# Kernel optimization log

Measured on AMD Instinct MI355X. Metric: run time of the kernel, lower is better.

The kernel has to match this reference:

```python
import jax, jax.numpy as jnp
import numpy as np

M, N, IN_DIM, NITER = 32, 32, 1024, 100
ALPHA, SIGMA = 0.3, 16.0  # sigma default = max(m, n) / 2
BATCH = 16384


def setup_inputs() -> dict:
    key = jax.random.key(0)
    k1, k2 = jax.random.split(key)
    x = jax.random.normal(k1, (BATCH, IN_DIM), dtype=jnp.float32)
    weights = jax.random.normal(k2, (IN_DIM, M * N), dtype=jnp.float32)
    ii, jj = jnp.meshgrid(jnp.arange(M), jnp.arange(N), indexing='ij')
    locations = jnp.stack([ii.ravel(), jj.ravel()], axis=1).astype(jnp.int32)  # (m*n, 2), row-major like the generator
    return {"x": x, "weights": weights, "locations": locations, "current_iter": 10}


def reference(x, weights, locations, current_iter):
    # x: (B, in_dim); weights: (in_dim, m*n); locations: (m*n, 2)
    B = x.shape[0]
    # Euclidean distances from each sample to each neuron, via ||a-b||^2 expansion
    x2 = jnp.sum(x * x, axis=1, keepdims=True)            # (B, 1)
    w2 = jnp.sum(weights * weights, axis=0)[None, :]      # (1, m*n)
    d2 = jnp.clip(x2 + w2 - 2.0 * (x @ weights), 0.0, None)
    dists = jnp.sqrt(d2)                                  # (B, m*n)
    loss_per = jnp.min(dists, axis=1)                     # (B,)
    bmu_index = jnp.argmin(dists, axis=1)                 # (B,)
    iter_correction = 1.0 - current_iter / NITER
    lr = ALPHA * iter_correction
    sigma = SIGMA * iter_correction
    loc_f = locations.astype(jnp.float32)                 # (m*n, 2)
    bmu_loc = loc_f[bmu_index]                            # (B, 2)
    # squared grid distance of every neuron to each sample's BMU
    dsq = jnp.sum((loc_f[None, :, :] - bmu_loc[:, None, :]) ** 2, axis=2)  # (B, m*n)
    lr_locations = jnp.exp(-dsq / (sigma * sigma)) * lr   # (B, m*n)
    # delta[i,k] = (1/B) * sum_b lr_locations[b,k] * (x[b,i] - weights[i,k])
    # computed without materializing the (B, in_dim, m*n) broadcast tensor
    pos = jnp.einsum('bk,bi->ik', lr_locations, x)        # (in_dim, m*n)
    neg = weights * jnp.sum(lr_locations, axis=0)[None, :]
    delta = (pos - neg) / B
    new_weights = weights + delta
    loss = jnp.sum(loss_per) / B
    return loss, new_weights
```

## Files before the change

kernel.cpp:

```cpp
#include <hip/hip_runtime.h>

typedef unsigned short u16;
typedef short bf16x8 __attribute__((ext_vector_type(8)));
typedef float f32x4 __attribute__((ext_vector_type(4)));

#define BATCH   16384
#define INDIM   1024
#define KNEUR   1024

__device__ __forceinline__ u16 f2bf(float f) {
  union { float f; unsigned u; } v; v.f = f;
  unsigned r = v.u + 0x7FFFu + ((v.u >> 16) & 1u);
  return (u16)(r >> 16);
}
__device__ __forceinline__ float bf2f(u16 h) {
  union { unsigned u; float f; } v; v.u = ((unsigned)h) << 16; return v.f;
}

#define GLDS(gp, lp) __builtin_amdgcn_global_load_lds( \
  (const __attribute__((address_space(1))) void*)(gp), \
  (__attribute__((address_space(3))) void*)(lp), 16, 0, 0)

__global__ void k_T(const int* __restrict__ loc, const int* __restrict__ itp,
                    u16* __restrict__ Tb, float* __restrict__ Tf,
                    float* __restrict__ Xf, int* __restrict__ cntcur,
                    float* __restrict__ S, float* __restrict__ w2) {
  int id = blockIdx.x * 256 + threadIdx.x;
  int c = id >> 10, k = id & 1023;
  float corr = 1.f - (float)itp[0] / 100.f;
  float lr = 0.3f * corr;
  float sig = 16.f * corr;
  float inv_s2 = 1.f / (sig * sig);
  int di = loc[2 * c] - loc[2 * k];
  int dj = loc[2 * c + 1] - loc[2 * k + 1];
  float v = lr * __expf(-(float)(di * di + dj * dj) * inv_s2);
  Tf[id] = v;
  Tb[id] = f2bf(v);
  Xf[id] = 0.f;
  if (id < 2048) cntcur[id] = 0;
  if (id < 1024) { S[id] = 0.f; w2[id] = 0.f; }
}

__global__ void k_conv_x(const float* __restrict__ x, u16* __restrict__ xb,
                         float* __restrict__ x2) {
  int b = blockIdx.x;
  int t = threadIdx.x;
  const float4 v = *(const float4*)(x + (size_t)b * INDIM + t * 4);
  u16 o0 = f2bf(v.x), o1 = f2bf(v.y), o2 = f2bf(v.z), o3 = f2bf(v.w);
  ushort4 o; o.x = o0; o.y = o1; o.z = o2; o.w = o3;
  *(ushort4*)(xb + (size_t)b * INDIM + t * 4) = o;
  float s = v.x * v.x + v.y * v.y + v.z * v.z + v.w * v.w;
  for (int m = 32; m; m >>= 1) s += __shfl_xor(s, m, 64);
  __shared__ float ws_[4];
  if ((t & 63) == 0) ws_[t >> 6] = s;
  __syncthreads();
  if (t == 0) x2[b] = ws_[0] + ws_[1] + ws_[2] + ws_[3];
}

__global__ void k_prepw(const float* __restrict__ w, u16* __restrict__ wt,
                        float* __restrict__ w2) {
  __shared__ float tile[64][65];
  __shared__ float red[4][64];
  int bi = blockIdx.x & 15;
  int bj = blockIdx.x >> 4;
  int tx = threadIdx.x & 63, ty = threadIdx.x >> 6;
  int i0 = bj * 64, k0 = bi * 64;
  float sq = 0.f;
  for (int r = ty; r < 64; r += 4) {
    float v = w[(size_t)(i0 + r) * KNEUR + k0 + tx];
    tile[r][tx] = v;
  }
  __syncthreads();
  for (int r = ty; r < 64; r += 4) {
    float v = tile[r][tx];
    sq += v * v;
  }
  red[ty][tx] = sq;
  for (int r = ty; r < 64; r += 4)
    wt[(size_t)(k0 + r) * INDIM + i0 + tx] = f2bf(tile[tx][r]);
  __syncthreads();
  if (ty == 0)
    atomicAdd(&w2[k0 + tx], red[0][tx] + red[1][tx] + red[2][tx] + red[3][tx]);
}

template <int EPI>
__global__ __launch_bounds__(256, 4)
void k_gemm(const u16* __restrict__ A, const u16* __restrict__ Bm,
            const float* __restrict__ x2, const float* __restrict__ w2,
            float* __restrict__ pmin, int* __restrict__ pidx,
            float* __restrict__ P4) {
  __shared__ __align__(16) u16 ldsA[128 * 64];
  __shared__ __align__(16) u16 ldsB[128 * 64];
  __shared__ float s_rv[2][128];
  __shared__ int   s_ri[2][128];

  int bid = blockIdx.x;
  int mb, nb, ktlo, kthi, ks;
  if (EPI == 1) {
    int swz = (bid & 7) * 128 + (bid >> 3);
    mb = swz >> 3; nb = swz & 7;
    ktlo = 0; kthi = 16; ks = 0;
  } else {
    ks = bid & 3;
    int tile = bid >> 2;
    mb = tile >> 3; nb = tile & 7;
    ktlo = ks * 4; kthi = ktlo + 4;
  }
  int lane = threadIdx.x & 63;
  int wid = threadIdx.x >> 6;
  int wr = wid >> 1, wc = wid & 1;

  f32x4 acc[4][4];
  #pragma unroll
  for (int i = 0; i < 4; ++i)
    #pragma unroll
    for (int j = 0; j < 4; ++j) { acc[i][j][0] = 0.f; acc[i][j][1] = 0.f; acc[i][j][2] = 0.f; acc[i][j][3] = 0.f; }

  const size_t rowA0 = (size_t)mb * 128;
  const size_t rowB0 = (size_t)nb * 128;

  for (int kt = ktlo; kt < kthi; ++kt) {
    int k0 = kt * 64;
    __syncthreads();
    #pragma unroll
    for (int q = 0; q < 4; ++q) {
      int p = q * 256 + wid * 64 + lane;
      int row = p >> 3;
      int clog = (p & 7) ^ (row & 7);
      GLDS(A + (rowA0 + row) * 1024 + k0 + clog * 8,
           ldsA + (size_t)(q * 256 + wid * 64) * 8);
    }
    #pragma unroll
    for (int q = 0; q < 4; ++q) {
      int p = q * 256 + wid * 64 + lane;
      int row = p >> 3;
      int clog = (p & 7) ^ (row & 7);
      GLDS(Bm + (rowB0 + row) * 1024 + k0 + clog * 8,
           ldsB + (size_t)(q * 256 + wid * 64) * 8);
    }
    __syncthreads();
    #pragma unroll
    for (int kk = 0; kk < 2; ++kk) {
      bf16x8 af[4], bfr[4];
      #pragma unroll
      for (int mt = 0; mt < 4; ++mt) {
        int row = wr * 64 + mt * 16 + (lane & 15);
        int ch = (kk * 4 + (lane >> 4)) ^ (row & 7);
        af[mt] = *(const bf16x8*)(ldsA + row * 64 + ch * 8);
      }
      #pragma unroll
      for (int nt = 0; nt < 4; ++nt) {
        int row = wc * 64 + nt * 16 + (lane & 15);
        int ch = (kk * 4 + (lane >> 4)) ^ (row & 7);
        bfr[nt] = *(const bf16x8*)(ldsB + row * 64 + ch * 8);
      }
      #pragma unroll
      for (int mt = 0; mt < 4; ++mt)
        #pragma unroll
        for (int nt = 0; nt < 4; ++nt)
          acc[mt][nt] = __builtin_amdgcn_mfma_f32_16x16x32_bf16(af[mt], bfr[nt], acc[mt][nt], 0, 0, 0);
    }
  }

  if (EPI == 1) {
    int g = lane >> 4;
    int li = lane & 15;
    #pragma unroll
    for (int mt = 0; mt < 4; ++mt) {
      #pragma unroll
      for (int r = 0; r < 4; ++r) {
        int rowl = wr * 64 + mt * 16 + g * 4 + r;
        float xv = x2[rowA0 + rowl];
        float v = 1e30f; int vi = 0;
        #pragma unroll
        for (int nt = 0; nt < 4; ++nt) {
          int col = (int)rowB0 + wc * 64 + nt * 16 + li;
          float d2 = xv + w2[col] - 2.f * acc[mt][nt][r];
          if (d2 < v) { v = d2; vi = col; }
        }
        #pragma unroll
        for (int m = 1; m < 16; m <<= 1) {
          float ov = __shfl_xor(v, m, 64);
          int oi = __shfl_xor(vi, m, 64);
          if (ov < v || (ov == v && oi < vi)) { v = ov; vi = oi; }
        }
        if (li == 0) { s_rv[wc][rowl] = v; s_ri[wc][rowl] = vi; }
      }
    }
    __syncthreads();
    int t = threadIdx.x;
    if (t < 128) {
      float v0 = s_rv[0][t], v1 = s_rv[1][t];
      int i0 = s_ri[0][t], i1 = s_ri[1][t];
      float v = v0; int vi = i0;
      if (v1 < v0) { v = v1; vi = i1; }
      size_t brow = rowA0 + t;
      pmin[brow * 8 + nb] = v;
      pidx[brow * 8 + nb] = vi;
    }
  } else {
    float* base = P4 + ((size_t)ks << 20);
    #pragma unroll
    for (int mt = 0; mt < 4; ++mt)
      #pragma unroll
      for (int nt = 0; nt < 4; ++nt)
        #pragma unroll
        for (int r = 0; r < 4; ++r) {
          int i = (int)rowA0 + wr * 64 + mt * 16 + (lane >> 4) * 4 + r;
          int k = (int)rowB0 + wc * 64 + nt * 16 + (lane & 15);
          base[(size_t)i * KNEUR + k] = acc[mt][nt][r];
        }
  }
}

__global__ void k_bmu_count(const float* __restrict__ pmin, const int* __restrict__ pidx,
                            int* __restrict__ bmu, float* __restrict__ lpart,
                            int* __restrict__ cnt) {
  int b = blockIdx.x * 256 + threadIdx.x;
  float v = 1e30f; int vi = 0;
  #pragma unroll
  for (int j = 0; j < 8; ++j) {
    float pv = pmin[(size_t)b * 8 + j];
    if (pv < v) { v = pv; vi = pidx[(size_t)b * 8 + j]; }
  }
  bmu[b] = vi;
  atomicAdd(&cnt[vi], 1);
  float d = sqrtf(fmaxf(v, 0.f));
  __shared__ float red[256];
  red[threadIdx.x] = d;
  __syncthreads();
  for (int s = 128; s > 0; s >>= 1) {
    if (threadIdx.x < s) red[threadIdx.x] += red[threadIdx.x + s];
    __syncthreads();
  }
  if (threadIdx.x == 0) lpart[blockIdx.x] = red[0];
}

__global__ void k_offsets_loss(const int* __restrict__ cntcur_in, int* __restrict__ cursor,
                               float* __restrict__ cntf,
                               const float* __restrict__ lpart, float* __restrict__ out) {
  __shared__ int s[1024];
  int t = threadIdx.x;
  int v = cntcur_in[t];
  cntf[t] = (float)v;
  s[t] = v;
  __syncthreads();
  for (int off = 1; off < 1024; off <<= 1) {
    int a = s[t];
    int b = (t >= off) ? s[t - off] : 0;
    __syncthreads();
    s[t] = a + b;
    __syncthreads();
  }
  cursor[t] = s[t] - v;
  if (t < 64) {
    float l = lpart[t];
    for (int m = 32; m; m >>= 1) l += __shfl_xor(l, m, 64);
    if (t == 0) out[0] = l * (1.f / (float)BATCH);
  }
}

__global__ void k_place(const int* __restrict__ bmu, int* __restrict__ cursor,
                        int* __restrict__ perm) {
  int b = blockIdx.x * 256 + threadIdx.x;
  int c = bmu[b];
  int p = atomicAdd(&cursor[c], 1);
  perm[p] = b;
}

__global__ __launch_bounds__(256)
void k_xsum2(const int* __restrict__ perm, const int* __restrict__ bmu,
             const u16* __restrict__ xb, float* __restrict__ Xf) {
  int t = threadIdx.x;
  int m0 = blockIdx.x * 16;
  int pm[16], cl[16];
  #pragma unroll
  for (int j = 0; j < 16; ++j) pm[j] = perm[m0 + j];
  #pragma unroll
  for (int j = 0; j < 16; ++j) cl[j] = bmu[pm[j]];
  float a0 = 0.f, a1 = 0.f, a2 = 0.f, a3 = 0.f;
  int ccur = cl[0];
  #pragma unroll
  for (int j = 0; j < 16; ++j) {
    if (cl[j] != ccur) {
      float* p = Xf + (size_t)ccur * INDIM + 4 * t;
      atomicAdd(p + 0, a0); atomicAdd(p + 1, a1);
      atomicAdd(p + 2, a2); atomicAdd(p + 3, a3);
      a0 = a1 = a2 = a3 = 0.f;
      ccur = cl[j];
    }
    ushort4 v = *(const ushort4*)(xb + (size_t)pm[j] * INDIM + t * 4);
    a0 += bf2f(v.x); a1 += bf2f(v.y); a2 += bf2f(v.z); a3 += bf2f(v.w);
  }
  float* p = Xf + (size_t)ccur * INDIM + 4 * t;
  atomicAdd(p + 0, a0); atomicAdd(p + 1, a1);
  atomicAdd(p + 2, a2); atomicAdd(p + 3, a3);
}

__global__ void k_xst_trans(const float* __restrict__ Xf, u16* __restrict__ xst) {
  __shared__ float tile[64][65];
  int bc = blockIdx.x & 15;
  int bi = blockIdx.x >> 4;
  int tx = threadIdx.x & 63, ty = threadIdx.x >> 6;
  int c0 = bc * 64, i0 = bi * 64;
  for (int r = ty; r < 64; r += 4)
    tile[r][tx] = Xf[(size_t)(c0 + r) * INDIM + i0 + tx];
  __syncthreads();
  for (int r = ty; r < 64; r += 4)
    xst[(size_t)(i0 + r) * KNEUR + c0 + tx] = f2bf(tile[tx][r]);
}

__global__ void k_S(const float* __restrict__ cntf, const float* __restrict__ Tf,
                    float* __restrict__ S) {
  int cchunk = blockIdx.x >> 2;
  int kb = blockIdx.x & 3;
  int k = kb * 256 + threadIdx.x;
  float s = 0.f;
  for (int c = cchunk * 64; c < cchunk * 64 + 64; ++c)
    s += cntf[c] * Tf[(size_t)c * KNEUR + k];
  atomicAdd(&S[k], s);
}

__global__ void k_wupd(const float* __restrict__ P4, const float* __restrict__ Wf,
                       const float* __restrict__ S, float* __restrict__ outw) {
  const float invB = 1.f / (float)BATCH;
  int id4 = blockIdx.x * 256 + threadIdx.x;
  size_t base = (size_t)id4 * 4;
  int k = (int)(base & 1023);
  float4 p0 = *(const float4*)(P4 + base);
  float4 p1 = *(const float4*)(P4 + (1u << 20) + base);
  float4 p2 = *(const float4*)(P4 + (2u << 20) + base);
  float4 p3 = *(const float4*)(P4 + (3u << 20) + base);
  float4 wv = *(const float4*)(Wf + base);
  float4 sv = *(const float4*)(S + k);
  outw[base + 0] = wv.x + (p0.x + p1.x + p2.x + p3.x - wv.x * sv.x) * invB;
  outw[base + 1] = wv.y + (p0.y + p1.y + p2.y + p3.y - wv.y * sv.y) * invB;
  outw[base + 2] = wv.z + (p0.z + p1.z + p2.z + p3.z - wv.z * sv.z) * invB;
  outw[base + 3] = wv.w + (p0.w + p1.w + p2.w + p3.w - wv.w * sv.w) * invB;
}

extern "C" void kernel_launch(void* const* d_in, const int* in_sizes, int n_in,
                              void* d_out, int out_size, void* d_ws, size_t ws_size,
                              hipStream_t stream) {
  const float* x = (const float*)d_in[0];
  const float* w = (const float*)d_in[1];
  const int* loc = (const int*)d_in[2];
  const int* it = (const int*)d_in[3];
  float* out = (float*)d_out;

  char* ws = (char*)d_ws;
  size_t off = 0;
  auto alloc = [&](size_t bytes) -> void* {
    void* p = ws + off;
    off += (bytes + 255) & ~(size_t)255;
    return p;
  };
  u16* xb    = (u16*)  alloc((size_t)BATCH * INDIM * 2);
  u16* wt    = (u16*)  alloc((size_t)KNEUR * INDIM * 2);
  u16* Tb    = (u16*)  alloc((size_t)KNEUR * KNEUR * 2);
  float* Tf  = (float*)alloc((size_t)KNEUR * KNEUR * 4);
  u16* xst   = (u16*)  alloc((size_t)INDIM * KNEUR * 2);
  float* x2  = (float*)alloc((size_t)BATCH * 4);
  float* w2  = (float*)alloc((size_t)KNEUR * 4);
  float* pmin= (float*)alloc((size_t)BATCH * 8 * 4);
  int* pidx  = (int*)  alloc((size_t)BATCH * 8 * 4);
  int* bmu   = (int*)  alloc((size_t)BATCH * 4);
  float* cntf= (float*)alloc((size_t)KNEUR * 4);
  float* S   = (float*)alloc((size_t)KNEUR * 4);
  float* lpart=(float*)alloc(64 * 4);
  float* Xf  = (float*)alloc((size_t)KNEUR * INDIM * 4);
  int* cntcur= (int*)  alloc((size_t)2 * KNEUR * 4);
  int* perm  = (int*)  alloc((size_t)BATCH * 4);
  if (off > ws_size) return;

  int* cnt = cntcur;
  int* cursor = cntcur + KNEUR;
  float* P4 = (float*)xb;

  k_T<<<4096, 256, 0, stream>>>(loc, it, Tb, Tf, Xf, cntcur, S, w2);
  k_conv_x<<<BATCH, 256, 0, stream>>>(x, xb, x2);
  k_prepw<<<256, 256, 0, stream>>>(w, wt, w2);
  k_gemm<1><<<1024, 256, 0, stream>>>(xb, wt, x2, w2, pmin, pidx, nullptr);
  k_bmu_count<<<64, 256, 0, stream>>>(pmin, pidx, bmu, lpart, cnt);
  k_offsets_loss<<<1, 1024, 0, stream>>>(cnt, cursor, cntf, lpart, out);
  k_place<<<64, 256, 0, stream>>>(bmu, cursor, perm);
  k_xsum2<<<BATCH / 16, 256, 0, stream>>>(perm, bmu, xb, Xf);
  k_xst_trans<<<256, 256, 0, stream>>>(Xf, xst);
  k_S<<<64, 256, 0, stream>>>(cntf, Tf, S);
  k_gemm<2><<<256, 256, 0, stream>>>(xst, Tb, nullptr, nullptr, nullptr, nullptr, P4);
  k_wupd<<<1024, 256, 0, stream>>>(P4, w, S, out + 1);
}
```

Baseline: 166.8 us.

## Merge prep kernels and middle stages into cooperative kernel, fuse weight update into GEMM

Folds the three prep kernels into one multi-role launch and moves the BMU, scan, place, x-sum, transpose and S stages into a single cooperative kernel that uses grid syncs in place of separate launches. The W*(1-S/B) base term is now written inside the cooperative kernel, and the second GEMM atomically adds its split-K partials scaled by 1/B straight into the output, so the P4 buffer and the final update kernel go away. w2 is now computed by dedicated column-reduction blocks rather than atomics. This removes launch gaps and a large scratch round trip, in exchange for grid-sync cost, float atomics on a 1M-element output, and a requirement that 1024 blocks can be co-resident.

```diff
diff --git a/kernel.cpp b/kernel.cpp
--- a/kernel.cpp
+++ b/kernel.cpp
@@ -1,4 +1,7 @@
 #include <hip/hip_runtime.h>
+#include <hip/hip_cooperative_groups.h>
+
+namespace cg = cooperative_groups;
 
 typedef unsigned short u16;
 typedef short bf16x8 __attribute__((ext_vector_type(8)));
@@ -21,66 +24,68 @@
   (const __attribute__((address_space(1))) void*)(gp), \
   (__attribute__((address_space(3))) void*)(lp), 16, 0, 0)
 
-__global__ void k_T(const int* __restrict__ loc, const int* __restrict__ itp,
-                    u16* __restrict__ Tb, float* __restrict__ Tf,
-                    float* __restrict__ Xf, int* __restrict__ cntcur,
-                    float* __restrict__ S, float* __restrict__ w2) {
-  int id = blockIdx.x * 256 + threadIdx.x;
-  int c = id >> 10, k = id & 1023;
-  float corr = 1.f - (float)itp[0] / 100.f;
-  float lr = 0.3f * corr;
-  float sig = 16.f * corr;
-  float inv_s2 = 1.f / (sig * sig);
-  int di = loc[2 * c] - loc[2 * k];
-  int dj = loc[2 * c + 1] - loc[2 * k + 1];
-  float v = lr * __expf(-(float)(di * di + dj * dj) * inv_s2);
-  Tf[id] = v;
-  Tb[id] = f2bf(v);
-  Xf[id] = 0.f;
-  if (id < 2048) cntcur[id] = 0;
-  if (id < 1024) { S[id] = 0.f; w2[id] = 0.f; }
-}
-
-__global__ void k_conv_x(const float* __restrict__ x, u16* __restrict__ xb,
-                         float* __restrict__ x2) {
-  int b = blockIdx.x;
-  int t = threadIdx.x;
-  const float4 v = *(const float4*)(x + (size_t)b * INDIM + t * 4);
-  u16 o0 = f2bf(v.x), o1 = f2bf(v.y), o2 = f2bf(v.z), o3 = f2bf(v.w);
-  ushort4 o; o.x = o0; o.y = o1; o.z = o2; o.w = o3;
-  *(ushort4*)(xb + (size_t)b * INDIM + t * 4) = o;
-  float s = v.x * v.x + v.y * v.y + v.z * v.z + v.w * v.w;
-  for (int m = 32; m; m >>= 1) s += __shfl_xor(s, m, 64);
-  __shared__ float ws_[4];
-  if ((t & 63) == 0) ws_[t >> 6] = s;
-  __syncthreads();
-  if (t == 0) x2[b] = ws_[0] + ws_[1] + ws_[2] + ws_[3];
-}
-
-__global__ void k_prepw(const float* __restrict__ w, u16* __restrict__ wt,
-                        float* __restrict__ w2) {
+__global__ __launch_bounds__(256)
+void k_prep(const float* __restrict__ x, u16* __restrict__ xb, float* __restrict__ x2,
+            const float* __restrict__ w, u16* __restrict__ wt, float* __restrict__ w2,
+            const int* __restrict__ loc, const int* __restrict__ itp,
+            u16* __restrict__ Tb, float* __restrict__ Tf,
+            float* __restrict__ Xf, int* __restrict__ cntcur) {
   __shared__ float tile[64][65];
   __shared__ float red[4][64];
-  int bi = blockIdx.x & 15;
-  int bj = blockIdx.x >> 4;
-  int tx = threadIdx.x & 63, ty = threadIdx.x >> 6;
-  int i0 = bj * 64, k0 = bi * 64;
-  float sq = 0.f;
-  for (int r = ty; r < 64; r += 4) {
-    float v = w[(size_t)(i0 + r) * KNEUR + k0 + tx];
-    tile[r][tx] = v;
-  }
-  __syncthreads();
-  for (int r = ty; r < 64; r += 4) {
-    float v = tile[r][tx];
-    sq += v * v;
-  }
-  red[ty][tx] = sq;
-  for (int r = ty; r < 64; r += 4)
-    wt[(size_t)(k0 + r) * INDIM + i0 + tx] = f2bf(tile[tx][r]);
-  __syncthreads();
-  if (ty == 0)
-    atomicAdd(&w2[k0 + tx], red[0][tx] + red[1][tx] + red[2][tx] + red[3][tx]);
+  int bid = blockIdx.x;
+  int t = threadIdx.x;
+  if (bid < 4096) {
+    int row = bid * 4 + (t >> 6);
+    int l = t & 63;
+    const float* xr = x + (size_t)row * INDIM;
+    u16* xbr = xb + (size_t)row * INDIM;
+    float s = 0.f;
+    #pragma unroll
+    for (int seg = 0; seg < 4; ++seg) {
+      float4 v = *(const float4*)(xr + seg * 256 + l * 4);
+      ushort4 o; o.x = f2bf(v.x); o.y = f2bf(v.y); o.z = f2bf(v.z); o.w = f2bf(v.w);
+      *(ushort4*)(xbr + seg * 256 + l * 4) = o;
+      s += v.x * v.x + v.y * v.y + v.z * v.z + v.w * v.w;
+    }
+    for (int m = 32; m; m >>= 1) s += __shfl_xor(s, m, 64);
+    if (l == 0) x2[row] = s;
+  } else if (bid < 8192) {
+    int id = (bid - 4096) * 256 + t;
+    int c = id >> 10, k = id & 1023;
+    float corr = 1.f - (float)itp[0] / 100.f;
+    float lr = 0.3f * corr;
+    float sig = 16.f * corr;
+    float inv_s2 = 1.f / (sig * sig);
+    int di = loc[2 * c] - loc[2 * k];
+    int dj = loc[2 * c + 1] - loc[2 * k + 1];
+    float v = lr * __expf(-(float)(di * di + dj * dj) * inv_s2);
+    Tf[id] = v;
+    Tb[id] = f2bf(v);
+    Xf[id] = 0.f;
+    if (id < 2048) cntcur[id] = 0;
+  } else if (bid < 8448) {
+    int bb = bid - 8192;
+    int bi = bb & 15;
+    int bj = bb >> 4;
+    int tx = t & 63, ty = t >> 6;
+    int i0 = bj * 64, k0 = bi * 64;
+    for (int r = ty; r < 64; r += 4)
+      tile[r][tx] = w[(size_t)(i0 + r) * KNEUR + k0 + tx];
+    __syncthreads();
+    for (int r = ty; r < 64; r += 4)
+      wt[(size_t)(k0 + r) * INDIM + i0 + tx] = f2bf(tile[tx][r]);
+  } else {
+    int tx = t & 63, ty = t >> 6;
+    int k = (bid - 8448) * 64 + tx;
+    float s = 0.f;
+    for (int i = ty * 256; i < ty * 256 + 256; ++i) {
+      float v = w[(size_t)i * KNEUR + k];
+      s += v * v;
+    }
+    red[ty][tx] = s;
+    __syncthreads();
+    if (ty == 0) w2[k] = red[0][tx] + red[1][tx] + red[2][tx] + red[3][tx];
+  }
 }
 
 template <int EPI>
@@ -88,20 +93,20 @@
 void k_gemm(const u16* __restrict__ A, const u16* __restrict__ Bm,
             const float* __restrict__ x2, const float* __restrict__ w2,
             float* __restrict__ pmin, int* __restrict__ pidx,
-            float* __restrict__ P4) {
+            float* __restrict__ outw) {
   __shared__ __align__(16) u16 ldsA[128 * 64];
   __shared__ __align__(16) u16 ldsB[128 * 64];
   __shared__ float s_rv[2][128];
   __shared__ int   s_ri[2][128];
 
   int bid = blockIdx.x;
-  int mb, nb, ktlo, kthi, ks;
+  int mb, nb, ktlo, kthi;
   if (EPI == 1) {
     int swz = (bid & 7) * 128 + (bid >> 3);
     mb = swz >> 3; nb = swz & 7;
-    ktlo = 0; kthi = 16; ks = 0;
+    ktlo = 0; kthi = 16;
   } else {
-    ks = bid & 3;
+    int ks = bid & 3;
     int tile = bid >> 2;
     mb = tile >> 3; nb = tile & 7;
     ktlo = ks * 4; kthi = ktlo + 4;
@@ -199,7 +204,7 @@
       pidx[brow * 8 + nb] = vi;
     }
   } else {
-    float* base = P4 + ((size_t)ks << 20);
+    const float invB = 1.f / (float)BATCH;
     #pragma unroll
     for (int mt = 0; mt < 4; ++mt)
       #pragma unroll
@@ -208,135 +213,138 @@
         for (int r = 0; r < 4; ++r) {
           int i = (int)rowA0 + wr * 64 + mt * 16 + (lane >> 4) * 4 + r;
           int k = (int)rowB0 + wc * 64 + nt * 16 + (lane & 15);
-          base[(size_t)i * KNEUR + k] = acc[mt][nt][r];
+          atomicAdd(&outw[(size_t)i * KNEUR + k], acc[mt][nt][r] * invB);
         }
   }
 }
 
-__global__ void k_bmu_count(const float* __restrict__ pmin, const int* __restrict__ pidx,
-                            int* __restrict__ bmu, float* __restrict__ lpart,
-                            int* __restrict__ cnt) {
-  int b = blockIdx.x * 256 + threadIdx.x;
-  float v = 1e30f; int vi = 0;
-  #pragma unroll
-  for (int j = 0; j < 8; ++j) {
-    float pv = pmin[(size_t)b * 8 + j];
-    if (pv < v) { v = pv; vi = pidx[(size_t)b * 8 + j]; }
-  }
-  bmu[b] = vi;
-  atomicAdd(&cnt[vi], 1);
-  float d = sqrtf(fmaxf(v, 0.f));
-  __shared__ float red[256];
-  red[threadIdx.x] = d;
-  __syncthreads();
-  for (int s = 128; s > 0; s >>= 1) {
-    if (threadIdx.x < s) red[threadIdx.x] += red[threadIdx.x + s];
-    __syncthreads();
-  }
-  if (threadIdx.x == 0) lpart[blockIdx.x] = red[0];
-}
-
-__global__ void k_offsets_loss(const int* __restrict__ cntcur_in, int* __restrict__ cursor,
-                               float* __restrict__ cntf,
-                               const float* __restrict__ lpart, float* __restrict__ out) {
-  __shared__ int s[1024];
+__global__ __launch_bounds__(256, 4)
+void k_coop(const float* __restrict__ pmin, const int* __restrict__ pidx,
+            int* __restrict__ bmu, float* __restrict__ lpart,
+            int* __restrict__ cnt, int* __restrict__ cursor,
+            float* __restrict__ cntf, float* __restrict__ out,
+            const u16* __restrict__ xb, int* __restrict__ perm,
+            float* __restrict__ Xf, u16* __restrict__ xst,
+            const float* __restrict__ Tf, float* __restrict__ S,
+            const float* __restrict__ w, float* __restrict__ outw) {
+  cg::grid_group grid = cg::this_grid();
+  int bid = blockIdx.x;
   int t = threadIdx.x;
-  int v = cntcur_in[t];
-  cntf[t] = (float)v;
-  s[t] = v;
-  __syncthreads();
-  for (int off = 1; off < 1024; off <<= 1) {
-    int a = s[t];
-    int b = (t >= off) ? s[t - off] : 0;
-    __syncthreads();
-    s[t] = a + b;
-    __syncthreads();
-  }
-  cursor[t] = s[t] - v;
-  if (t < 64) {
-    float l = lpart[t];
-    for (int m = 32; m; m >>= 1) l += __shfl_xor(l, m, 64);
-    if (t == 0) out[0] = l * (1.f / (float)BATCH);
-  }
-}
-
-__global__ void k_place(const int* __restrict__ bmu, int* __restrict__ cursor,
-                        int* __restrict__ perm) {
-  int b = blockIdx.x * 256 + threadIdx.x;
-  int c = bmu[b];
-  int p = atomicAdd(&cursor[c], 1);
-  perm[p] = b;
-}
-
-__global__ __launch_bounds__(256)
-void k_xsum2(const int* __restrict__ perm, const int* __restrict__ bmu,
-             const u16* __restrict__ xb, float* __restrict__ Xf) {
-  int t = threadIdx.x;
-  int m0 = blockIdx.x * 16;
-  int pm[16], cl[16];
-  #pragma unroll
-  for (int j = 0; j < 16; ++j) pm[j] = perm[m0 + j];
-  #pragma unroll
-  for (int j = 0; j < 16; ++j) cl[j] = bmu[pm[j]];
-  float a0 = 0.f, a1 = 0.f, a2 = 0.f, a3 = 0.f;
-  int ccur = cl[0];
-  #pragma unroll
-  for (int j = 0; j < 16; ++j) {
-    if (cl[j] != ccur) {
-      float* p = Xf + (size_t)ccur * INDIM + 4 * t;
-      atomicAdd(p + 0, a0); atomicAdd(p + 1, a1);
-      atomicAdd(p + 2, a2); atomicAdd(p + 3, a3);
-      a0 = a1 = a2 = a3 = 0.f;
-      ccur = cl[j];
-    }
-    ushort4 v = *(const ushort4*)(xb + (size_t)pm[j] * INDIM + t * 4);
-    a0 += bf2f(v.x); a1 += bf2f(v.y); a2 += bf2f(v.z); a3 += bf2f(v.w);
-  }
-  float* p = Xf + (size_t)ccur * INDIM + 4 * t;
-  atomicAdd(p + 0, a0); atomicAdd(p + 1, a1);
-  atomicAdd(p + 2, a2); atomicAdd(p + 3, a3);
-}
-
-__global__ void k_xst_trans(const float* __restrict__ Xf, u16* __restrict__ xst) {
   __shared__ float tile[64][65];
-  int bc = blockIdx.x & 15;
-  int bi = blockIdx.x >> 4;
-  int tx = threadIdx.x & 63, ty = threadIdx.x >> 6;
-  int c0 = bc * 64, i0 = bi * 64;
-  for (int r = ty; r < 64; r += 4)
-    tile[r][tx] = Xf[(size_t)(c0 + r) * INDIM + i0 + tx];
-  __syncthreads();
-  for (int r = ty; r < 64; r += 4)
-    xst[(size_t)(i0 + r) * KNEUR + c0 + tx] = f2bf(tile[tx][r]);
-}
-
-__global__ void k_S(const float* __restrict__ cntf, const float* __restrict__ Tf,
-                    float* __restrict__ S) {
-  int cchunk = blockIdx.x >> 2;
-  int kb = blockIdx.x & 3;
-  int k = kb * 256 + threadIdx.x;
-  float s = 0.f;
-  for (int c = cchunk * 64; c < cchunk * 64 + 64; ++c)
-    s += cntf[c] * Tf[(size_t)c * KNEUR + k];
-  atomicAdd(&S[k], s);
-}
-
-__global__ void k_wupd(const float* __restrict__ P4, const float* __restrict__ Wf,
-                       const float* __restrict__ S, float* __restrict__ outw) {
-  const float invB = 1.f / (float)BATCH;
-  int id4 = blockIdx.x * 256 + threadIdx.x;
-  size_t base = (size_t)id4 * 4;
-  int k = (int)(base & 1023);
-  float4 p0 = *(const float4*)(P4 + base);
-  float4 p1 = *(const float4*)(P4 + (1u << 20) + base);
-  float4 p2 = *(const float4*)(P4 + (2u << 20) + base);
-  float4 p3 = *(const float4*)(P4 + (3u << 20) + base);
-  float4 wv = *(const float4*)(Wf + base);
-  float4 sv = *(const float4*)(S + k);
-  outw[base + 0] = wv.x + (p0.x + p1.x + p2.x + p3.x - wv.x * sv.x) * invB;
-  outw[base + 1] = wv.y + (p0.y + p1.y + p2.y + p3.y - wv.y * sv.y) * invB;
-  outw[base + 2] = wv.z + (p0.z + p1.z + p2.z + p3.z - wv.z * sv.z) * invB;
-  outw[base + 3] = wv.w + (p0.w + p1.w + p2.w + p3.w - wv.w * sv.w) * invB;
+
+  if (bid < 64) {
+    int b = bid * 256 + t;
+    float v = 1e30f; int vi = 0;
+    #pragma unroll
+    for (int j = 0; j < 8; ++j) {
+      float pv = pmin[(size_t)b * 8 + j];
+      if (pv < v) { v = pv; vi = pidx[(size_t)b * 8 + j]; }
+    }
+    bmu[b] = vi;
+    atomicAdd(&cnt[vi], 1);
+    float d = sqrtf(fmaxf(v, 0.f));
+    __shared__ float red[256];
+    red[t] = d;
+    __syncthreads();
+    for (int s = 128; s > 0; s >>= 1) {
+      if (t < s) red[t] += red[t + s];
+      __syncthreads();
+    }
+    if (t == 0) lpart[bid] = red[0];
+  }
+  grid.sync();
+
+  if (bid == 0) {
+    __shared__ int sc[256];
+    int4 c4 = *(const int4*)(cnt + 4 * t);
+    int tsum = c4.x + c4.y + c4.z + c4.w;
+    sc[t] = tsum;
+    __syncthreads();
+    for (int off = 1; off < 256; off <<= 1) {
+      int val = sc[t];
+      int add = (t >= off) ? sc[t - off] : 0;
+      __syncthreads();
+      sc[t] = val + add;
+      __syncthreads();
+    }
+    int excl = sc[t] - tsum;
+    cursor[4 * t + 0] = excl;
+    cursor[4 * t + 1] = excl + c4.x;
+    cursor[4 * t + 2] = excl + c4.x + c4.y;
+    cursor[4 * t + 3] = excl + c4.x + c4.y + c4.z;
+    cntf[4 * t + 0] = (float)c4.x;
+    cntf[4 * t + 1] = (float)c4.y;
+    cntf[4 * t + 2] = (float)c4.z;
+    cntf[4 * t + 3] = (float)c4.w;
+    if (t < 64) {
+      float l = lpart[t];
+      for (int m = 32; m; m >>= 1) l += __shfl_xor(l, m, 64);
+      if (t == 0) out[0] = l * (1.f / (float)BATCH);
+    }
+  }
+  grid.sync();
+
+  if (bid < 64) {
+    int b = bid * 256 + t;
+    int c = bmu[b];
+    int p = atomicAdd(&cursor[c], 1);
+    perm[p] = b;
+  } else if (bid < 68) {
+    int k = (bid - 64) * 256 + t;
+    float s = 0.f;
+    for (int c = 0; c < KNEUR; ++c)
+      s += cntf[c] * Tf[(size_t)c * KNEUR + k];
+    S[k] = s;
+  }
+  grid.sync();
+
+  {
+    int m0 = bid * 16;
+    int pm[16], cl[16];
+    #pragma unroll
+    for (int j = 0; j < 16; ++j) pm[j] = perm[m0 + j];
+    #pragma unroll
+    for (int j = 0; j < 16; ++j) cl[j] = bmu[pm[j]];
+    float a0 = 0.f, a1 = 0.f, a2 = 0.f, a3 = 0.f;
+    int ccur = cl[0];
+    #pragma unroll
+    for (int j = 0; j < 16; ++j) {
+      if (cl[j] != ccur) {
+        float* p = Xf + (size_t)ccur * INDIM + 4 * t;
+        atomicAdd(p + 0, a0); atomicAdd(p + 1, a1);
+        atomicAdd(p + 2, a2); atomicAdd(p + 3, a3);
+        a0 = a1 = a2 = a3 = 0.f;
+        ccur = cl[j];
+      }
+      ushort4 v = *(const ushort4*)(xb + (size_t)pm[j] * INDIM + t * 4);
+      a0 += bf2f(v.x); a1 += bf2f(v.y); a2 += bf2f(v.z); a3 += bf2f(v.w);
+    }
+    float* p = Xf + (size_t)ccur * INDIM + 4 * t;
+    atomicAdd(p + 0, a0); atomicAdd(p + 1, a1);
+    atomicAdd(p + 2, a2); atomicAdd(p + 3, a3);
+  }
+  grid.sync();
+
+  if (bid < 256) {
+    int bc = bid & 15;
+    int bi = bid >> 4;
+    int tx = t & 63, ty = t >> 6;
+    int c0 = bc * 64, i0 = bi * 64;
+    for (int r = ty; r < 64; r += 4)
+      tile[r][tx] = Xf[(size_t)(c0 + r) * INDIM + i0 + tx];
+    __syncthreads();
+    for (int r = ty; r < 64; r += 4)
+      xst[(size_t)(i0 + r) * KNEUR + c0 + tx] = f2bf(tile[tx][r]);
+  } else if (bid < 512) {
+    const float invB = 1.f / (float)BATCH;
+    size_t base = ((size_t)(bid - 256) * 256 + t) * 16;
+    int k = (int)(base & 1023);
+    #pragma unroll
+    for (int j = 0; j < 16; ++j) {
+      float wv = w[base + j];
+      outw[base + j] = wv - wv * S[k + j] * invB;
+    }
+  }
 }
 
 extern "C" void kernel_launch(void* const* d_in, const int* in_sizes, int n_in,
@@ -375,18 +383,28 @@
 
   int* cnt = cntcur;
   int* cursor = cntcur + KNEUR;
-  float* P4 = (float*)xb;
-
-  k_T<<<4096, 256, 0, stream>>>(loc, it, Tb, Tf, Xf, cntcur, S, w2);
-  k_conv_x<<<BATCH, 256, 0, stream>>>(x, xb, x2);
-  k_prepw<<<256, 256, 0, stream>>>(w, wt, w2);
+  float* outw = out + 1;
+
+  k_prep<<<8464, 256, 0, stream>>>(x, xb, x2, w, wt, w2, loc, it, Tb, Tf, Xf, cntcur);
   k_gemm<1><<<1024, 256, 0, stream>>>(xb, wt, x2, w2, pmin, pidx, nullptr);
-  k_bmu_count<<<64, 256, 0, stream>>>(pmin, pidx, bmu, lpart, cnt);
-  k_offsets_loss<<<1, 1024, 0, stream>>>(cnt, cursor, cntf, lpart, out);
-  k_place<<<64, 256, 0, stream>>>(bmu, cursor, perm);
-  k_xsum2<<<BATCH / 16, 256, 0, stream>>>(perm, bmu, xb, Xf);
-  k_xst_trans<<<256, 256, 0, stream>>>(Xf, xst);
-  k_S<<<64, 256, 0, stream>>>(cntf, Tf, S);
-  k_gemm<2><<<256, 256, 0, stream>>>(xst, Tb, nullptr, nullptr, nullptr, nullptr, P4);
-  k_wupd<<<1024, 256, 0, stream>>>(P4, w, S, out + 1);
-}
+
+  {
+    const float* a_pmin = pmin; const int* a_pidx = pidx;
+    int* a_bmu = bmu; float* a_lpart = lpart;
+    int* a_cnt = cnt; int* a_cursor = cursor;
+    float* a_cntf = cntf; float* a_out = out;
+    const u16* a_xb = xb; int* a_perm = perm;
+    float* a_Xf = Xf; u16* a_xst = xst;
+    const float* a_Tf = Tf; float* a_S = S;
+    const float* a_w = w; float* a_outw = outw;
+    void* args[16] = {
+      (void*)&a_pmin, (void*)&a_pidx, (void*)&a_bmu, (void*)&a_lpart,
+      (void*)&a_cnt, (void*)&a_cursor, (void*)&a_cntf, (void*)&a_out,
+      (void*)&a_xb, (void*)&a_perm, (void*)&a_Xf, (void*)&a_xst,
+      (void*)&a_Tf, (void*)&a_S, (void*)&a_w, (void*)&a_outw
+    };
+    hipLaunchCooperativeKernel((void*)k_coop, dim3(1024), dim3(256), args, 0, stream);
+  }
+
+  k_gemm<2><<<256, 256, 0, stream>>>(xst, Tb, nullptr, nullptr, nullptr, nullptr, outw);
+}
```

Result: slower. 590.9 us (+254.3%).
